# Kernel optimization log

Measured on AMD Instinct MI355X. Metric: run time of the kernel, lower is better.

The kernel has to match this reference:

```python
import jax, jax.numpy as jnp
import numpy as np

B, T, E, V, A = 8192, 64, 128, 32000, 10


def setup_inputs() -> dict:
    key = jax.random.key(0)
    ks = jax.random.split(key, 8)
    return {
        "utterance": jax.random.randint(ks[0], (B, T), 0, V + 1, dtype=jnp.int64)
            if jax.config.jax_enable_x64 else jax.random.randint(ks[0], (B, T), 0, V + 1).astype(jnp.int32),
        "global_idxes": jnp.arange(B, dtype=jnp.int32),
        "emb_table": jax.random.normal(ks[1], (V + 1, E), jnp.float32) * 0.1,
        "w_ih": jax.random.normal(ks[2], (3 * E, E), jnp.float32) * 0.1,
        "w_hh": jax.random.normal(ks[3], (3 * E, E), jnp.float32) * 0.1,
        "b_ih": jax.random.normal(ks[4], (3 * E,), jnp.float32) * 0.1,
        "b_hh": jax.random.normal(ks[5], (3 * E,), jnp.float32) * 0.1,
        "w_out": jax.random.normal(ks[6], (A, E), jnp.float32) * 0.1,
        "b_out": jax.random.normal(ks[7], (A,), jnp.float32) * 0.1,
    }


def _gru_cell(x, h, w_ih, w_hh, b_ih, b_hh):
    # PyTorch GRUCell math
    gi = x @ w_ih.T + b_ih  # [B, 3E]
    gh = h @ w_hh.T + b_hh  # [B, 3E]
    i_r, i_z, i_n = jnp.split(gi, 3, axis=-1)
    h_r, h_z, h_n = jnp.split(gh, 3, axis=-1)
    r = jax.nn.sigmoid(i_r + h_r)
    z = jax.nn.sigmoid(i_z + h_z)
    n = jnp.tanh(i_n + r * h_n)
    return (1.0 - z) * n + z * h


def reference(utterance, global_idxes, emb_table, w_ih, w_hh, b_ih, b_hh, w_out, b_out):
    bsz = utterance.shape[0]
    h0 = jnp.zeros((bsz, emb_table.shape[1]), emb_table.dtype)
    alive0 = jnp.ones((bsz,), jnp.bool_)

    def step(carry, tok):
        h, out, alive = carry
        emb = emb_table[tok]                      # [B, E] gather
        h = _gru_cell(emb, h, w_ih, w_hh, b_ih, b_hh)
        # output_state only written for rows still alive entering this step
        out = jnp.where(alive[:, None], h, out)
        alive = alive & (tok != 0)                # mark_dead AFTER writing state
        return (h, out, alive), None

    tokens = utterance.T                          # [T, B]
    (_, out_state, _), _ = jax.lax.scan(step, (h0, h0, alive0), tokens)
    logits = out_state @ w_out.T + b_out          # [B, A]
    action_probs = jax.nn.softmax(logits, axis=-1)
    return action_probs
```

## Files before the change

kernel.cpp:

```cpp
#include <hip/hip_runtime.h>
#include <hip/hip_fp16.h>

#define Tt 64
#define Ee 128
#define Aa 10
#define Vv 32001

typedef __attribute__((ext_vector_type(8))) _Float16 half8;
typedef __attribute__((ext_vector_type(4))) _Float16 half4;
typedef __attribute__((ext_vector_type(4))) float f32x4;

#define L2E 1.44269504f

__device__ __forceinline__ float fast_rcp(float x) { return __builtin_amdgcn_rcpf(x); }
__device__ __forceinline__ float fast_exp2(float x) {
#if __has_builtin(__builtin_amdgcn_exp2f)
    return __builtin_amdgcn_exp2f(x);
#else
    return __expf(x * 0.69314718056f);
#endif
}

__device__ __forceinline__ half8 load_h8(const float* p) {
    f32x4 a = *(const f32x4*)p;
    f32x4 b = *(const f32x4*)(p + 4);
    half8 r;
    r[0] = (_Float16)a[0]; r[1] = (_Float16)a[1]; r[2] = (_Float16)a[2]; r[3] = (_Float16)a[3];
    r[4] = (_Float16)b[0]; r[5] = (_Float16)b[1]; r[6] = (_Float16)b[2]; r[7] = (_Float16)b[3];
    return r;
}
__device__ __forceinline__ half8 load_h8s(const float* p, float s) {
    f32x4 a = *(const f32x4*)p;
    f32x4 b = *(const f32x4*)(p + 4);
    half8 r;
#pragma unroll
    for (int j = 0; j < 4; ++j) { r[j] = (_Float16)(a[j] * s); r[4 + j] = (_Float16)(b[j] * s); }
    return r;
}

#define MFMA_F16(a, b, c)  __builtin_amdgcn_mfma_f32_16x16x32_f16(a, b, c, 0, 0, 0)

__global__ __launch_bounds__(512, 2) void gi_precompute(
    const float* __restrict__ emb, const float* __restrict__ w_ih,
    const float* __restrict__ b_ih, const float* __restrict__ b_hh,
    char* __restrict__ gw) {
    __shared__ __align__(16) char xs[8192];
    const int tid = threadIdx.x;
    const int wv = tid >> 6;
    const int ln = tid & 63;
    const int fn = ln & 15;
    const int kg = ln >> 4;
    const int v0 = blockIdx.x * 32;
    const int gc = wv * 16 + fn;
    const int srow = tid >> 4;
    const int c8 = (tid & 15) << 3;

    {
        int v = v0 + srow; if (v >= Vv) v = Vv - 1;
        half8 hx = load_h8(emb + (size_t)v * Ee + c8);
        int off = (srow * 256 + c8 * 2) ^ ((srow & 7) << 4);
        *(half8*)(xs + off) = hx;
    }
    half8 wr[4], wz[4], wn[4];
#pragma unroll
    for (int kt = 0; kt < 4; ++kt) {
        int k0 = kt * 32 + kg * 8;
        wr[kt] = load_h8(w_ih + (size_t)gc * Ee + k0);
        wz[kt] = load_h8(w_ih + (size_t)(128 + gc) * Ee + k0);
        wn[kt] = load_h8(w_ih + (size_t)(256 + gc) * Ee + k0);
    }
    const float bcr = b_ih[gc] + b_hh[gc];
    const float bcz = b_ih[128 + gc] + b_hh[128 + gc];
    const float bcn = b_ih[256 + gc];
    __syncthreads();

    f32x4 ar[2], az[2], an[2];
#pragma unroll
    for (int mt = 0; mt < 2; ++mt) {
        ar[mt] = (f32x4){0.f, 0.f, 0.f, 0.f};
        az[mt] = (f32x4){0.f, 0.f, 0.f, 0.f};
        an[mt] = (f32x4){0.f, 0.f, 0.f, 0.f};
    }
#pragma unroll
    for (int kt = 0; kt < 4; ++kt)
#pragma unroll
        for (int mt = 0; mt < 2; ++mt) {
            int r = mt * 16 + fn;
            int off = (r * 256 + (kt * 32 + kg * 8) * 2) ^ ((r & 7) << 4);
            half8 ha = *(const half8*)(xs + off);
            ar[mt] = MFMA_F16(ha, wr[kt], ar[mt]);
            az[mt] = MFMA_F16(ha, wz[kt], az[mt]);
            an[mt] = MFMA_F16(ha, wn[kt], an[mt]);
        }
#pragma unroll
    for (int mt = 0; mt < 2; ++mt)
#pragma unroll
        for (int i = 0; i < 4; ++i) {
            int v = v0 + mt * 16 + kg * 4 + i;
            if (v < Vv) {
                half4 g;
                g[0] = (_Float16)((ar[mt][i] + bcr) * (-L2E));
                g[1] = (_Float16)((az[mt][i] + bcz) * (-L2E));
                g[2] = (_Float16)((an[mt][i] + bcn) * (2.f * L2E));
                g[3] = (_Float16)0.f;
                *(half4*)(gw + (size_t)v * 1024 + gc * 8) = g;
            }
        }
}

#define SM_BYTES 26240

struct GateState {
    f32x4 h, o;
    int ts[4];
    half4 g[4];
};

__device__ __forceinline__ void gates_one(
    const f32x4& ar, const f32x4& az, const f32x4& an,
    GateState& st, int s, char* wbase, const int* wof, bool wr) {
#pragma unroll
    for (int i = 0; i < 4; ++i) {
        float ea = fast_exp2(ar[i]);
        float eb = fast_exp2(az[i]);
        float da = 1.f + ea, db = 1.f + eb;
        float R = fast_rcp(da * db);
        float rr = db * R;
        float zz = da * R;
        float pnp = (float)st.g[i][2] + rr * an[i];
        float ec = fast_exp2(pnp);
        float nn = 1.f - 2.f * fast_rcp(ec + 1.f);
        float h = nn + zz * (st.h[i] - nn);
        st.h[i] = h;
        if (s == st.ts[i]) st.o[i] = h;
        if (wr) *(_Float16*)(wbase + wof[i]) = (_Float16)h;
    }
}

__global__ __launch_bounds__(512, 1) void gru_dual_kernel(
    const int* __restrict__ utt, const char* __restrict__ gwc,
    const float* __restrict__ w_hh, const float* __restrict__ b_hh,
    const float* __restrict__ w_out, const float* __restrict__ b_out,
    float* __restrict__ out) {
    __shared__ __align__(16) char smem[SM_BYTES];
    int* tokb = (int*)smem;
    float* lg = (float*)(smem + 24576);
    int* tstar = (int*)(smem + 26112);
    float* outst = (float*)(smem + 8192);

    const int tid = threadIdx.x;
    const int wv = tid >> 6;
    const int ln = tid & 63;
    const int fn = ln & 15;
    const int kg = ln >> 4;
    const int row0 = blockIdx.x * 32;
    const int gc = wv * 16 + fn;
    const int gc8 = gc * 8;

    if (tid < 32) tstar[tid] = Tt - 1;
    *(float2*)(smem + 8192 + tid * 8) = (float2){0.f, 0.f};
    *(float2*)(smem + 16384 + tid * 8) = (float2){0.f, 0.f};
    __syncthreads();
    {
        int4 tv = ((const int4*)(utt + (size_t)row0 * Tt))[tid];
        int4 sv = {tv.x << 10, tv.y << 10, tv.z << 10, tv.w << 10};
        ((int4*)tokb)[tid] = sv;
        int row = tid >> 4;
        int tq = (tid & 15) << 2;
        if (tv.x == 0) atomicMin(&tstar[row], tq);
        if (tv.y == 0) atomicMin(&tstar[row], tq + 1);
        if (tv.z == 0) atomicMin(&tstar[row], tq + 2);
        if (tv.w == 0) atomicMin(&tstar[row], tq + 3);
    }
    half8 whr[4], whz[4], whn[4];
#pragma unroll
    for (int kt = 0; kt < 4; ++kt) {
        int k0 = kt * 32 + kg * 8;
        whr[kt] = load_h8s(w_hh + (size_t)gc * Ee + k0, -L2E);
        whz[kt] = load_h8s(w_hh + (size_t)(128 + gc) * Ee + k0, -L2E);
        whn[kt] = load_h8s(w_hh + (size_t)(256 + gc) * Ee + k0, 2.f * L2E);
    }
    const float bhn2 = b_hh[256 + gc] * (2.f * L2E);
    __syncthreads();

    int offk[4], wof[4];
#pragma unroll
    for (int kt = 0; kt < 4; ++kt)
        offk[kt] = (fn * 256 + (kt * 32 + kg * 8) * 2) ^ ((fn & 7) << 4);
#pragma unroll
    for (int i = 0; i < 4; ++i) {
        int row = kg * 4 + i;
        wof[i] = (row * 256 + gc * 2) ^ ((row & 7) << 4);
    }

    GateState A, B;
#pragma unroll
    for (int i = 0; i < 4; ++i) {
        A.h[i] = 0.f; A.o[i] = 0.f; B.h[i] = 0.f; B.o[i] = 0.f;
        A.ts[i] = tstar[kg * 4 + i];
        B.ts[i] = tstar[16 + kg * 4 + i];
        A.g[i] = *(const half4*)(gwc + (tokb[(kg * 4 + i) * 64] + gc8));
        B.g[i] = *(const half4*)(gwc + (tokb[(16 + kg * 4 + i) * 64] + gc8));
    }

#pragma unroll 1
    for (int k = 0; k < Tt; ++k) {
        const char* hA = smem + 8192 + (k & 1) * 4096;
        const char* hB = smem + 16384 + (k & 1) * 4096;
        half8 fA[4], fB[4];
#pragma unroll
        for (int kt = 0; kt < 4; ++kt) fA[kt] = *(const half8*)(hA + offk[kt]);
#pragma unroll
        for (int kt = 0; kt < 4; ++kt) fB[kt] = *(const half8*)(hB + offk[kt]);
        int t2 = (k < Tt - 1) ? k + 1 : Tt - 1;
        half4 gnxA[4], gnxB[4];
#pragma unroll
        for (int i = 0; i < 4; ++i) {
            gnxA[i] = *(const half4*)(gwc + (tokb[(kg * 4 + i) * 64 + t2] + gc8));
            gnxB[i] = *(const half4*)(gwc + (tokb[(16 + kg * 4 + i) * 64 + t2] + gc8));
        }
        f32x4 arA, azA, anA, arB, azB, anB;
#pragma unroll
        for (int i = 0; i < 4; ++i) {
            arA[i] = (float)A.g[i][0]; azA[i] = (float)A.g[i][1]; anA[i] = bhn2;
            arB[i] = (float)B.g[i][0]; azB[i] = (float)B.g[i][1]; anB[i] = bhn2;
        }
        __builtin_amdgcn_s_setprio(1);
#pragma unroll
        for (int kt = 0; kt < 4; ++kt) {
            arA = MFMA_F16(fA[kt], whr[kt], arA);
            azA = MFMA_F16(fA[kt], whz[kt], azA);
            anA = MFMA_F16(fA[kt], whn[kt], anA);
        }
#pragma unroll
        for (int kt = 0; kt < 4; ++kt) {
            arB = MFMA_F16(fB[kt], whr[kt], arB);
            azB = MFMA_F16(fB[kt], whz[kt], azB);
            anB = MFMA_F16(fB[kt], whn[kt], anB);
        }
        __builtin_amdgcn_s_setprio(0);

        char* wA = smem + 8192 + ((k + 1) & 1) * 4096;
        char* wB = smem + 16384 + ((k + 1) & 1) * 4096;
        bool wr = (k < Tt - 1);
        gates_one(arA, azA, anA, A, k, wA, wof, wr);
        gates_one(arB, azB, anB, B, k, wB, wof, wr);
#pragma unroll
        for (int i = 0; i < 4; ++i) { A.g[i] = gnxA[i]; B.g[i] = gnxB[i]; }
        if (k < Tt - 1) {
            __builtin_amdgcn_sched_barrier(0);
            asm volatile("s_waitcnt lgkmcnt(0)" ::: "memory");
            __builtin_amdgcn_s_barrier();
            __builtin_amdgcn_sched_barrier(0);
        }
    }

    __syncthreads();
#pragma unroll
    for (int i = 0; i < 4; ++i) {
        outst[(kg * 4 + i) * Ee + gc] = A.o[i];
        outst[(16 + kg * 4 + i) * Ee + gc] = B.o[i];
    }
    __syncthreads();

    if (tid < 32 * Aa) {
        int r = tid / Aa, a = tid % Aa;
        const float* wo = w_out + a * Ee;
        const float* os = outst + r * Ee;
        float s = b_out[a];
#pragma unroll
        for (int j = 0; j < Ee; j += 4) {
            f32x4 o = *(const f32x4*)(os + j);
            f32x4 w4 = *(const f32x4*)(wo + j);
            s += o[0] * w4[0] + o[1] * w4[1] + o[2] * w4[2] + o[3] * w4[3];
        }
        lg[r * 12 + a] = s;
    }
    __syncthreads();
    if (tid < 32) {
        float v[Aa];
        float mx = -1e30f;
#pragma unroll
        for (int a = 0; a < Aa; ++a) {
            v[a] = lg[tid * 12 + a];
            mx = fmaxf(mx, v[a]);
        }
        float sum = 0.f;
#pragma unroll
        for (int a = 0; a < Aa; ++a) {
            v[a] = __expf(v[a] - mx);
            sum += v[a];
        }
        float inv = fast_rcp(sum);
#pragma unroll
        for (int a = 0; a < Aa; ++a) out[(size_t)(row0 + tid) * Aa + a] = v[a] * inv;
    }
}

#define FSM_BYTES 21312
__global__ __launch_bounds__(512, 2) void gru_fallback_kernel(
    const int* __restrict__ utt, const float* __restrict__ emb,
    const float* __restrict__ w_ih, const float* __restrict__ w_hh,
    const float* __restrict__ b_ih, const float* __restrict__ b_hh,
    const float* __restrict__ w_out, const float* __restrict__ b_out,
    float* __restrict__ out) {
    __shared__ __align__(16) char smem[FSM_BYTES];
    int* tokb = (int*)smem;
    float* lg = (float*)(smem + 20480);
    int* tstar = (int*)(smem + 21248);
    float* outst = (float*)(smem + 4096);

    const int tid = threadIdx.x;
    const int wv = tid >> 6;
    const int ln = tid & 63;
    const int fn = ln & 15;
    const int kg = ln >> 4;
    const int row0 = blockIdx.x * 16;
    const int gc = wv * 16 + fn;
    const int srow = tid >> 5;
    const int c4 = (tid & 31) << 2;

    if (tid < 16) tstar[tid] = Tt - 1;
    *(float2*)(smem + 12288 + tid * 8) = (float2){0.f, 0.f};
    __syncthreads();
    {
        int2 tv = ((const int2*)(utt + (size_t)row0 * Tt))[tid];
        ((int2*)tokb)[tid] = tv;
        int row = tid >> 5;
        int tq = (tid & 31) << 1;
        if (tv.x == 0) atomicMin(&tstar[row], tq);
        if (tv.y == 0) atomicMin(&tstar[row], tq + 1);
    }
    half8 wir[4], wiz[4], win[4], whr[4], whz[4], whn[4];
#pragma unroll
    for (int kt = 0; kt < 4; ++kt) {
        int k0 = kt * 32 + kg * 8;
        wir[kt] = load_h8(w_ih + (size_t)gc * Ee + k0);
        wiz[kt] = load_h8(w_ih + (size_t)(128 + gc) * Ee + k0);
        win[kt] = load_h8(w_ih + (size_t)(256 + gc) * Ee + k0);
        whr[kt] = load_h8(w_hh + (size_t)gc * Ee + k0);
        whz[kt] = load_h8(w_hh + (size_t)(128 + gc) * Ee + k0);
        whn[kt] = load_h8(w_hh + (size_t)(256 + gc) * Ee + k0);
    }
    const float bcr = b_ih[gc] + b_hh[gc];
    const float bcz = b_ih[128 + gc] + b_hh[128 + gc];
    const float bin = b_ih[256 + gc];
    const float bhn = b_hh[256 + gc];
    __syncthreads();
    int ts[4];
#pragma unroll
    for (int i = 0; i < 4; ++i) ts[i] = tstar[kg * 4 + i];
    {
        int tok = tokb[srow * Tt];
        f32x4 a = *(const f32x4*)(emb + (size_t)tok * Ee + c4);
        half4 hx;
#pragma unroll
        for (int j = 0; j < 4; ++j) hx[j] = (_Float16)a[j];
        int off = (srow * 256 + c4 * 2) ^ ((srow & 7) << 4);
        *(half4*)(smem + 4096 + off) = hx;
    }
    __syncthreads();
    f32x4 hreg = (f32x4){0.f, 0.f, 0.f, 0.f};
    f32x4 oreg = (f32x4){0.f, 0.f, 0.f, 0.f};
    int cur = 0;
#pragma unroll 1
    for (int t = 0; t < Tt; ++t) {
        f32x4 pa;
        if (t < Tt - 1) {
            int tok = tokb[srow * Tt + t + 1];
            pa = *(const f32x4*)(emb + (size_t)tok * Ee + c4);
        }
        const char* xb = smem + 4096 + cur * 4096;
        const char* hb = smem + 12288 + cur * 4096;
        f32x4 ar = (f32x4){0.f, 0.f, 0.f, 0.f};
        f32x4 az = (f32x4){0.f, 0.f, 0.f, 0.f};
        f32x4 ain = (f32x4){0.f, 0.f, 0.f, 0.f};
        f32x4 ahn = (f32x4){0.f, 0.f, 0.f, 0.f};
        __builtin_amdgcn_s_setprio(1);
#pragma unroll
        for (int kt = 0; kt < 4; ++kt) {
            int off = (fn * 256 + (kt * 32 + kg * 8) * 2) ^ ((fn & 7) << 4);
            half8 xa = *(const half8*)(xb + off);
            half8 ha = *(const half8*)(hb + off);
            ar = MFMA_F16(xa, wir[kt], ar);
            ar = MFMA_F16(ha, whr[kt], ar);
            az = MFMA_F16(xa, wiz[kt], az);
            az = MFMA_F16(ha, whz[kt], az);
            ain = MFMA_F16(xa, win[kt], ain);
            ahn = MFMA_F16(ha, whn[kt], ahn);
        }
        __builtin_amdgcn_s_setprio(0);
        char* hn = smem + 12288 + (cur ^ 1) * 4096;
#pragma unroll
        for (int i = 0; i < 4; ++i) {
            float pr = ar[i] + bcr;
            float pz = az[i] + bcz;
            float rr = fast_rcp(1.f + __expf(-pr));
            float zz = fast_rcp(1.f + __expf(-pz));
            float pn = ain[i] + bin + rr * (ahn[i] + bhn);
            float e2 = __expf(2.f * pn);
            float nn = 1.f - 2.f * fast_rcp(e2 + 1.f);
            float h = (1.f - zz) * nn + zz * hreg[i];
            hreg[i] = h;
            if (t == ts[i]) oreg[i] = h;
            if (t < Tt - 1) {
                int row = kg * 4 + i;
                int off = (row * 256 + gc * 2) ^ ((row & 7) << 4);
                *(_Float16*)(hn + off) = (_Float16)h;
            }
        }
        if (t < Tt - 1) {
            half4 hx;
#pragma unroll
            for (int j = 0; j < 4; ++j) hx[j] = (_Float16)pa[j];
            int off = (srow * 256 + c4 * 2) ^ ((srow & 7) << 4);
            *(half4*)(smem + 4096 + (cur ^ 1) * 4096 + off) = hx;
        }
        __syncthreads();
        cur ^= 1;
    }
#pragma unroll
    for (int i = 0; i < 4; ++i) outst[(kg * 4 + i) * Ee + gc] = oreg[i];
    __syncthreads();
    if (tid < 16 * Aa) {
        int r = tid / Aa, a = tid % Aa;
        const float* wo = w_out + a * Ee;
        const float* os = outst + r * Ee;
        float s = b_out[a];
#pragma unroll
        for (int j = 0; j < Ee; j += 4) {
            f32x4 o = *(const f32x4*)(os + j);
            f32x4 w4 = *(const f32x4*)(wo + j);
            s += o[0] * w4[0] + o[1] * w4[1] + o[2] * w4[2] + o[3] * w4[3];
        }
        lg[r * 12 + a] = s;
    }
    __syncthreads();
    if (tid < 16) {
        float v[Aa];
        float mx = -1e30f;
#pragma unroll
        for (int a = 0; a < Aa; ++a) {
            v[a] = lg[tid * 12 + a];
            mx = fmaxf(mx, v[a]);
        }
        float sum = 0.f;
#pragma unroll
        for (int a = 0; a < Aa; ++a) {
            v[a] = __expf(v[a] - mx);
            sum += v[a];
        }
        float inv = fast_rcp(sum);
#pragma unroll
        for (int a = 0; a < Aa; ++a) out[(size_t)(row0 + tid) * Aa + a] = v[a] * inv;
    }
}

extern "C" void kernel_launch(void* const* d_in, const int* in_sizes, int n_in,
                              void* d_out, int out_size, void* d_ws, size_t ws_size,
                              hipStream_t stream) {
    (void)in_sizes; (void)n_in; (void)out_size;
    const int* utt = (const int*)d_in[0];
    const float* emb = (const float*)d_in[2];
    const float* wih = (const float*)d_in[3];
    const float* whh = (const float*)d_in[4];
    const float* bih = (const float*)d_in[5];
    const float* bhh = (const float*)d_in[6];
    const float* wout = (const float*)d_in[7];
    const float* bout = (const float*)d_in[8];
    const size_t need = (size_t)Vv * 1024;
    if (ws_size >= need) {
        char* gw = (char*)d_ws;
        gi_precompute<<<dim3((Vv + 31) / 32), 512, 0, stream>>>(emb, wih, bih, bhh, gw);
        gru_dual_kernel<<<256, 512, 0, stream>>>(utt, gw, whh, bhh, wout, bout, (float*)d_out);
    } else {
        gru_fallback_kernel<<<512, 512, 0, stream>>>(utt, emb, wih, whh, bih, bhh, wout, bout,
                                                     (float*)d_out);
    }
}
```

Baseline: 147.3 us.

## Repartition GRU recurrence to 16 rows per 256-thread block with 2 column tiles

The GRU recurrence kernel now processes 16 batch rows per block with 4 waves, and each wave covers two 16-column gate tiles instead of one. Before, each block held 32 rows as two independent row groups with 8 waves. This halves the number of threads that join each per-step barrier and gives each wave more independent MFMAs per step to interleave. The cost is twice as many weight registers per thread, and it relies on two blocks sharing a CU (launch bounds 256,2) to keep the same total occupancy with 512 blocks.

```diff
diff --git a/kernel.cpp b/kernel.cpp
--- a/kernel.cpp
+++ b/kernel.cpp
@@ -39,6 +39,11 @@
 }
 
 #define MFMA_F16(a, b, c)  __builtin_amdgcn_mfma_f32_16x16x32_f16(a, b, c, 0, 0, 0)
+
+#define BAR_LGKM() do { \
+    asm volatile("s_waitcnt lgkmcnt(0)" ::: "memory"); \
+    __builtin_amdgcn_s_barrier(); \
+} while (0)
 
 __global__ __launch_bounds__(512, 2) void gi_precompute(
     const float* __restrict__ emb, const float* __restrict__ w_ih,
@@ -108,58 +113,30 @@
         }
 }
 
-#define SM_BYTES 26240
-
-struct GateState {
-    f32x4 h, o;
-    int ts[4];
-    half4 g[4];
-};
-
-__device__ __forceinline__ void gates_one(
-    const f32x4& ar, const f32x4& az, const f32x4& an,
-    GateState& st, int s, char* wbase, const int* wof, bool wr) {
-#pragma unroll
-    for (int i = 0; i < 4; ++i) {
-        float ea = fast_exp2(ar[i]);
-        float eb = fast_exp2(az[i]);
-        float da = 1.f + ea, db = 1.f + eb;
-        float R = fast_rcp(da * db);
-        float rr = db * R;
-        float zz = da * R;
-        float pnp = (float)st.g[i][2] + rr * an[i];
-        float ec = fast_exp2(pnp);
-        float nn = 1.f - 2.f * fast_rcp(ec + 1.f);
-        float h = nn + zz * (st.h[i] - nn);
-        st.h[i] = h;
-        if (s == st.ts[i]) st.o[i] = h;
-        if (wr) *(_Float16*)(wbase + wof[i]) = (_Float16)h;
-    }
-}
-
-__global__ __launch_bounds__(512, 1) void gru_dual_kernel(
+#define SM_BYTES 13120
+
+__global__ __launch_bounds__(256, 2) void gru_quad_kernel(
     const int* __restrict__ utt, const char* __restrict__ gwc,
     const float* __restrict__ w_hh, const float* __restrict__ b_hh,
     const float* __restrict__ w_out, const float* __restrict__ b_out,
     float* __restrict__ out) {
     __shared__ __align__(16) char smem[SM_BYTES];
     int* tokb = (int*)smem;
-    float* lg = (float*)(smem + 24576);
-    int* tstar = (int*)(smem + 26112);
-    float* outst = (float*)(smem + 8192);
+    float* lg = (float*)(smem + 12288);
+    int* tstar = (int*)(smem + 13056);
+    float* outst = (float*)(smem + 4096);
 
     const int tid = threadIdx.x;
     const int wv = tid >> 6;
     const int ln = tid & 63;
     const int fn = ln & 15;
     const int kg = ln >> 4;
-    const int row0 = blockIdx.x * 32;
-    const int gc = wv * 16 + fn;
-    const int gc8 = gc * 8;
-
-    if (tid < 32) tstar[tid] = Tt - 1;
-    *(float2*)(smem + 8192 + tid * 8) = (float2){0.f, 0.f};
-    *(float2*)(smem + 16384 + tid * 8) = (float2){0.f, 0.f};
+    const int row0 = blockIdx.x * 16;
+    const int gc0 = wv * 32 + fn;
+    const int gc1 = gc0 + 16;
+
+    if (tid < 16) tstar[tid] = Tt - 1;
+    *(f32x4*)(smem + 4096 + tid * 16) = (f32x4){0.f, 0.f, 0.f, 0.f};
     __syncthreads();
     {
         int4 tv = ((const int4*)(utt + (size_t)row0 * Tt))[tid];
@@ -172,98 +149,123 @@
         if (tv.z == 0) atomicMin(&tstar[row], tq + 2);
         if (tv.w == 0) atomicMin(&tstar[row], tq + 3);
     }
-    half8 whr[4], whz[4], whn[4];
+    half8 whr[2][4], whz[2][4], whn[2][4];
 #pragma unroll
     for (int kt = 0; kt < 4; ++kt) {
         int k0 = kt * 32 + kg * 8;
-        whr[kt] = load_h8s(w_hh + (size_t)gc * Ee + k0, -L2E);
-        whz[kt] = load_h8s(w_hh + (size_t)(128 + gc) * Ee + k0, -L2E);
-        whn[kt] = load_h8s(w_hh + (size_t)(256 + gc) * Ee + k0, 2.f * L2E);
-    }
-    const float bhn2 = b_hh[256 + gc] * (2.f * L2E);
-    __syncthreads();
-
-    int offk[4], wof[4];
+        whr[0][kt] = load_h8s(w_hh + (size_t)gc0 * Ee + k0, -L2E);
+        whr[1][kt] = load_h8s(w_hh + (size_t)gc1 * Ee + k0, -L2E);
+        whz[0][kt] = load_h8s(w_hh + (size_t)(128 + gc0) * Ee + k0, -L2E);
+        whz[1][kt] = load_h8s(w_hh + (size_t)(128 + gc1) * Ee + k0, -L2E);
+        whn[0][kt] = load_h8s(w_hh + (size_t)(256 + gc0) * Ee + k0, 2.f * L2E);
+        whn[1][kt] = load_h8s(w_hh + (size_t)(256 + gc1) * Ee + k0, 2.f * L2E);
+    }
+    const float bhn2_0 = b_hh[256 + gc0] * (2.f * L2E);
+    const float bhn2_1 = b_hh[256 + gc1] * (2.f * L2E);
+    __syncthreads();
+
+    int offk[4], wof[2][4];
 #pragma unroll
     for (int kt = 0; kt < 4; ++kt)
         offk[kt] = (fn * 256 + (kt * 32 + kg * 8) * 2) ^ ((fn & 7) << 4);
 #pragma unroll
     for (int i = 0; i < 4; ++i) {
         int row = kg * 4 + i;
-        wof[i] = (row * 256 + gc * 2) ^ ((row & 7) << 4);
-    }
-
-    GateState A, B;
+        wof[0][i] = (row * 256 + gc0 * 2) ^ ((row & 7) << 4);
+        wof[1][i] = (row * 256 + gc1 * 2) ^ ((row & 7) << 4);
+    }
+
+    int ts[4];
+#pragma unroll
+    for (int i = 0; i < 4; ++i) ts[i] = tstar[kg * 4 + i];
+
+    half4 g0[4], g1[4];
 #pragma unroll
     for (int i = 0; i < 4; ++i) {
-        A.h[i] = 0.f; A.o[i] = 0.f; B.h[i] = 0.f; B.o[i] = 0.f;
-        A.ts[i] = tstar[kg * 4 + i];
-        B.ts[i] = tstar[16 + kg * 4 + i];
-        A.g[i] = *(const half4*)(gwc + (tokb[(kg * 4 + i) * 64] + gc8));
-        B.g[i] = *(const half4*)(gwc + (tokb[(16 + kg * 4 + i) * 64] + gc8));
-    }
+        int to = tokb[(kg * 4 + i) * 64];
+        g0[i] = *(const half4*)(gwc + to + gc0 * 8);
+        g1[i] = *(const half4*)(gwc + to + gc1 * 8);
+    }
+
+    f32x4 h0 = (f32x4){0.f, 0.f, 0.f, 0.f}, o0 = h0;
+    f32x4 h1 = h0, o1 = h0;
 
 #pragma unroll 1
     for (int k = 0; k < Tt; ++k) {
-        const char* hA = smem + 8192 + (k & 1) * 4096;
-        const char* hB = smem + 16384 + (k & 1) * 4096;
-        half8 fA[4], fB[4];
-#pragma unroll
-        for (int kt = 0; kt < 4; ++kt) fA[kt] = *(const half8*)(hA + offk[kt]);
-#pragma unroll
-        for (int kt = 0; kt < 4; ++kt) fB[kt] = *(const half8*)(hB + offk[kt]);
+        const char* hRd = smem + 4096 + (k & 1) * 4096;
+        char* hWr = smem + 4096 + ((k + 1) & 1) * 4096;
+        half8 f[4];
+#pragma unroll
+        for (int kt = 0; kt < 4; ++kt) f[kt] = *(const half8*)(hRd + offk[kt]);
         int t2 = (k < Tt - 1) ? k + 1 : Tt - 1;
-        half4 gnxA[4], gnxB[4];
-#pragma unroll
-        for (int i = 0; i < 4; ++i) {
-            gnxA[i] = *(const half4*)(gwc + (tokb[(kg * 4 + i) * 64 + t2] + gc8));
-            gnxB[i] = *(const half4*)(gwc + (tokb[(16 + kg * 4 + i) * 64 + t2] + gc8));
-        }
-        f32x4 arA, azA, anA, arB, azB, anB;
-#pragma unroll
-        for (int i = 0; i < 4; ++i) {
-            arA[i] = (float)A.g[i][0]; azA[i] = (float)A.g[i][1]; anA[i] = bhn2;
-            arB[i] = (float)B.g[i][0]; azB[i] = (float)B.g[i][1]; anB[i] = bhn2;
+        half4 gn0[4], gn1[4];
+#pragma unroll
+        for (int i = 0; i < 4; ++i) {
+            int to = tokb[(kg * 4 + i) * 64 + t2];
+            gn0[i] = *(const half4*)(gwc + to + gc0 * 8);
+            gn1[i] = *(const half4*)(gwc + to + gc1 * 8);
+        }
+        f32x4 ar0, az0, an0, ar1, az1, an1;
+#pragma unroll
+        for (int i = 0; i < 4; ++i) {
+            ar0[i] = (float)g0[i][0]; az0[i] = (float)g0[i][1]; an0[i] = bhn2_0;
+            ar1[i] = (float)g1[i][0]; az1[i] = (float)g1[i][1]; an1[i] = bhn2_1;
         }
         __builtin_amdgcn_s_setprio(1);
 #pragma unroll
         for (int kt = 0; kt < 4; ++kt) {
-            arA = MFMA_F16(fA[kt], whr[kt], arA);
-            azA = MFMA_F16(fA[kt], whz[kt], azA);
-            anA = MFMA_F16(fA[kt], whn[kt], anA);
-        }
-#pragma unroll
-        for (int kt = 0; kt < 4; ++kt) {
-            arB = MFMA_F16(fB[kt], whr[kt], arB);
-            azB = MFMA_F16(fB[kt], whz[kt], azB);
-            anB = MFMA_F16(fB[kt], whn[kt], anB);
+            ar0 = MFMA_F16(f[kt], whr[0][kt], ar0);
+            az0 = MFMA_F16(f[kt], whz[0][kt], az0);
+            an0 = MFMA_F16(f[kt], whn[0][kt], an0);
+            ar1 = MFMA_F16(f[kt], whr[1][kt], ar1);
+            az1 = MFMA_F16(f[kt], whz[1][kt], az1);
+            an1 = MFMA_F16(f[kt], whn[1][kt], an1);
         }
         __builtin_amdgcn_s_setprio(0);
-
-        char* wA = smem + 8192 + ((k + 1) & 1) * 4096;
-        char* wB = smem + 16384 + ((k + 1) & 1) * 4096;
         bool wr = (k < Tt - 1);
-        gates_one(arA, azA, anA, A, k, wA, wof, wr);
-        gates_one(arB, azB, anB, B, k, wB, wof, wr);
-#pragma unroll
-        for (int i = 0; i < 4; ++i) { A.g[i] = gnxA[i]; B.g[i] = gnxB[i]; }
-        if (k < Tt - 1) {
-            __builtin_amdgcn_sched_barrier(0);
-            asm volatile("s_waitcnt lgkmcnt(0)" ::: "memory");
-            __builtin_amdgcn_s_barrier();
-            __builtin_amdgcn_sched_barrier(0);
-        }
-    }
-
-    __syncthreads();
+#pragma unroll
+        for (int i = 0; i < 4; ++i) {
+            float ea = fast_exp2(ar0[i]);
+            float eb = fast_exp2(az0[i]);
+            float da = 1.f + ea, db = 1.f + eb;
+            float R = fast_rcp(da * db);
+            float rr = db * R, zz = da * R;
+            float pnp = (float)g0[i][2] + rr * an0[i];
+            float ec = fast_exp2(pnp);
+            float nn = 1.f - 2.f * fast_rcp(ec + 1.f);
+            float h = nn + zz * (h0[i] - nn);
+            h0[i] = h;
+            if (k == ts[i]) o0[i] = h;
+            if (wr) *(_Float16*)(hWr + wof[0][i]) = (_Float16)h;
+        }
+#pragma unroll
+        for (int i = 0; i < 4; ++i) {
+            float ea = fast_exp2(ar1[i]);
+            float eb = fast_exp2(az1[i]);
+            float da = 1.f + ea, db = 1.f + eb;
+            float R = fast_rcp(da * db);
+            float rr = db * R, zz = da * R;
+            float pnp = (float)g1[i][2] + rr * an1[i];
+            float ec = fast_exp2(pnp);
+            float nn = 1.f - 2.f * fast_rcp(ec + 1.f);
+            float h = nn + zz * (h1[i] - nn);
+            h1[i] = h;
+            if (k == ts[i]) o1[i] = h;
+            if (wr) *(_Float16*)(hWr + wof[1][i]) = (_Float16)h;
+        }
+#pragma unroll
+        for (int i = 0; i < 4; ++i) { g0[i] = gn0[i]; g1[i] = gn1[i]; }
+        BAR_LGKM();
+    }
+
 #pragma unroll
     for (int i = 0; i < 4; ++i) {
-        outst[(kg * 4 + i) * Ee + gc] = A.o[i];
-        outst[(16 + kg * 4 + i) * Ee + gc] = B.o[i];
-    }
-    __syncthreads();
-
-    if (tid < 32 * Aa) {
+        outst[(kg * 4 + i) * Ee + gc0] = o0[i];
+        outst[(kg * 4 + i) * Ee + gc1] = o1[i];
+    }
+    __syncthreads();
+
+    if (tid < 16 * Aa) {
         int r = tid / Aa, a = tid % Aa;
         const float* wo = w_out + a * Ee;
         const float* os = outst + r * Ee;
@@ -277,7 +279,7 @@
         lg[r * 12 + a] = s;
     }
     __syncthreads();
-    if (tid < 32) {
+    if (tid < 16) {
         float v[Aa];
         float mx = -1e30f;
 #pragma unroll
@@ -472,7 +474,7 @@
     if (ws_size >= need) {
         char* gw = (char*)d_ws;
         gi_precompute<<<dim3((Vv + 31) / 32), 512, 0, stream>>>(emb, wih, bih, bhh, gw);
-        gru_dual_kernel<<<256, 512, 0, stream>>>(utt, gw, whh, bhh, wout, bout, (float*)d_out);
+        gru_quad_kernel<<<512, 256, 0, stream>>>(utt, gw, whh, bhh, wout, bout, (float*)d_out);
     } else {
         gru_fallback_kernel<<<512, 512, 0, stream>>>(utt, emb, wih, whh, bih, bhh, wout, bout,
                                                      (float*)d_out);
```

After: 134.6 us. 8.6% less time.
